# Optimization experiments

Hardware: AMD Instinct MI355X
Metric: run time of the kernel (lower is better)

## Reference

```python
import jax, jax.numpy as jnp
import numpy as np
from jax import lax

# --- geometry constants (match init_kwargs geo) ---
NVOX = (128, 128, 128)          # (nz, ny, nx) voxels
SVOX = (256.0, 256.0, 256.0)    # volume size in mm
NDET = (256, 256)               # (V, U) detector pixels
SDET = (512.0, 512.0)           # detector size in mm
DSO = 1000.0                    # source-to-isocenter distance
DSD = 1536.0                    # source-to-detector distance
N_ANGLES = 360


def setup_inputs() -> dict:
    key = jax.random.key(0)
    # projections: [B, 1, n_angles, nDetV, nDetU]
    x = jax.random.normal(key, (2, 1, N_ANGLES, NDET[0], NDET[1]), dtype=jnp.float32)
    return {"x": x}


def _backproject(proj):
    """Voxel-driven cone-beam back-projection (adjoint of cone-beam forward projector).

    proj: [B, A, V, U] projections over a circular source trajectory.
    returns volume [B, nz, ny, nx].
    """
    B, A, V, U = proj.shape
    nz, ny, nx = NVOX
    dz, dy, dx = SVOX[0] / nz, SVOX[1] / ny, SVOX[2] / nx
    dv, du = SDET[0] / V, SDET[1] / U

    # voxel center coordinates (isocenter at origin)
    zc = ((jnp.arange(nz, dtype=jnp.float32) - (nz - 1) / 2) * dz)[:, None, None]  # [nz,1,1]
    yc = ((jnp.arange(ny, dtype=jnp.float32) - (ny - 1) / 2) * dy)[None, :, None]  # [1,ny,1]
    xc = ((jnp.arange(nx, dtype=jnp.float32) - (nx - 1) / 2) * dx)[None, None, :]  # [1,1,nx]

    angles = jnp.linspace(0.0, 2.0 * np.pi, A, endpoint=False, dtype=jnp.float32)
    proj_a = jnp.moveaxis(proj, 1, 0)  # [A, B, V, U] for scan over angles

    def bilinear(p, iv, iu):
        # p: [B, V, U]; iv, iu: [nz, ny, nx] fractional detector coords
        valid = (iu >= 0) & (iu <= U - 1) & (iv >= 0) & (iv <= V - 1)
        iu = jnp.clip(iu, 0.0, U - 1.0)
        iv = jnp.clip(iv, 0.0, V - 1.0)
        u0 = jnp.floor(iu).astype(jnp.int32)
        v0 = jnp.floor(iv).astype(jnp.int32)
        u1 = jnp.minimum(u0 + 1, U - 1)
        v1 = jnp.minimum(v0 + 1, V - 1)
        fu = iu - u0
        fv = iv - v0
        s = (p[:, v0, u0] * ((1 - fv) * (1 - fu))
             + p[:, v0, u1] * ((1 - fv) * fu)
             + p[:, v1, u0] * (fv * (1 - fu))
             + p[:, v1, u1] * (fv * fu))            # [B,nz,ny,nx]
        return s * valid.astype(p.dtype)

    def body(vol, inp):
        theta, p = inp                                # scalar, [B,V,U]
        c, s = jnp.cos(theta), jnp.sin(theta)
        xr = xc * c + yc * s                          # rotated in-plane coords [1,ny,nx]
        yr = -xc * s + yc * c                         # [1,ny,nx]
        mag = DSD / (DSO - xr)                        # perspective magnification [1,ny,nx]
        iu = jnp.broadcast_to(yr * mag / du + (U - 1) / 2, (nz, ny, nx))
        iv = zc * mag / dv + (V - 1) / 2              # [nz,ny,nx]
        vol = vol + bilinear(p, iv, iu)
        return vol, None

    vol0 = jnp.zeros((B, nz, ny, nx), dtype=proj.dtype)
    vol, _ = lax.scan(body, vol0, (angles, proj_a))
    return vol


def reference(x):
    # x: [B, 1, A, V, U] -> volume [B, 1, nz, ny, nx]
    vol = _backproject(x[:, 0])
    return vol[:, None]
```

## Files before the change

### kernel.cpp

```cpp
#include <hip/hip_runtime.h>
#include <math.h>

#define NA    360
#define ZPT   8
#define CROWS 24
#define CPITCH 52
#define NCELLP 1280
#define VLO_MAX 231
#define ULO_MAX 204
#define BSTRIDE 94371840


typedef float v2f __attribute__((ext_vector_type(2)));
typedef __attribute__((address_space(1))) const void gas_t;
typedef __attribute__((address_space(3))) void las_t;

__device__ __forceinline__ int2 bbox_angle(float c, float s,
    float xclo, float xchi, float yclo, float ychi, float zvlo, float zvhi)
{
    const float a0 = xclo*c, a1 = xchi*c, b0 = yclo*s, b1 = ychi*s;
    const float xr0 = a0+b0, xr1 = a0+b1, xr2 = a1+b0, xr3 = a1+b1;
    const float xmn = fminf(fminf(xr0,xr1), fminf(xr2,xr3));
    const float xmx = fmaxf(fmaxf(xr0,xr1), fmaxf(xr2,xr3));
    const float c0 = yclo*c, c1 = ychi*c, d0 = xclo*s, d1 = xchi*s;
    const float yr0 = c0-d0, yr1 = c0-d1, yr2 = c1-d0, yr3 = c1-d1;
    const float ymn = fminf(fminf(yr0,yr1), fminf(yr2,yr3));
    const float ymx = fmaxf(fmaxf(yr0,yr1), fmaxf(yr2,yr3));
    const float mlo = 1536.f * __builtin_amdgcn_rcpf(1000.f - xmn);
    const float mhi = 1536.f * __builtin_amdgcn_rcpf(1000.f - xmx);
    const float umn = fminf(fminf(ymn*mlo, ymn*mhi), fminf(ymx*mlo, ymx*mhi));
    int u_lo = (int)floorf(fmaf(umn, 0.5f, 127.5f)) - 1;
    u_lo = u_lo < 0 ? 0 : (u_lo > ULO_MAX ? ULO_MAX : u_lo);
    const float vmn = fminf(fminf(zvlo*mlo, zvlo*mhi), fminf(zvhi*mlo, zvhi*mhi));
    int v_lo = (int)floorf(vmn + 127.5f) - 1;
    v_lo = v_lo < 0 ? 0 : (v_lo > VLO_MAX ? VLO_MAX : v_lo);
    return make_int2(u_lo, v_lo);
}

__device__ __forceinline__ void stage10(const char* gb, float* ldsw,
                                        const int goffB[10]) {
    #pragma unroll
    for (int i = 0; i < 10; ++i) {
        __builtin_amdgcn_global_load_lds(
            (gas_t*)(gb + goffB[i]),
            (las_t*)(ldsw + i * 64), 4, 0, 0);
    }
}

__device__ __forceinline__ void compute_angle(const v2f* __restrict__ smb,
    float c, float s, float xc, float yc, float zf0, int u_lo, int v_lo,
    v2f acc[ZPT])
{
    const float xr  = xc*c + yc*s;
    const float yr  = yc*c - xc*s;
    const float mag = 1536.f * __builtin_amdgcn_rcpf(1000.f - xr);
    const float iu  = fmaf(yr*mag, 0.5f, 127.5f);
    const bool uval = (iu >= 0.f) && (iu <= 255.f);
    const float iuc = fminf(fmaxf(iu, 0.f), 255.f);
    int u0 = (int)iuc; u0 = u0 > 254 ? 254 : u0;
    const float fu  = iuc - (float)u0;
    const float w   = uval ? 1.f : 0.f;
    const float wu1 = fu*w, wu0 = w - wu1;
    const v2f   w0v = {wu0, wu0};
    const v2f   w1v = {wu1, wu1};
    const int   ui  = u0 - u_lo;
    const float ivb = fmaf(zf0, mag, 127.5f) - (float)v_lo;
    #pragma unroll
    for (int k = 0; k < ZPT; ++k) {
        const float ivl = fmaf((float)k, mag, ivb);
        const int   v0  = (int)ivl;
        const float fv  = __builtin_amdgcn_fractf(ivl);
        const v2f* cell = smb + (v0 * CPITCH + ui);
        const v2f c00 = cell[0];
        const v2f c10 = cell[CPITCH];
        const v2f c01 = cell[1];
        const v2f c11 = cell[CPITCH+1];
        const v2f fvv = {fv, fv};
        const v2f q0 = __builtin_elementwise_fma(fvv, c10 - c00, c00);
        const v2f q1 = __builtin_elementwise_fma(fvv, c11 - c01, c01);
        acc[k] = __builtin_elementwise_fma(w0v, q0, acc[k]);
        acc[k] = __builtin_elementwise_fma(w1v, q1, acc[k]);
    }
}

__global__ __launch_bounds__(256, 4) void bp_kernel(const float* __restrict__ proj,
                                                    float* __restrict__ out) {
    __shared__ float2 cs_sh[NA];
    __shared__ int2   bb_sh[NA];
    __shared__ v2f    patch[2][NCELLP];

    const int tid = threadIdx.y * 16 + threadIdx.x;

    const int zg = blockIdx.x;
    const int t  = blockIdx.y;
    const int x0 = (t & 7) * 16;
    const int y0 = (t >> 3) * 16;
    const int zb = zg * ZPT;

    const float zf0  = (float)zb - 63.5f;
    const float xclo = ((float)x0 - 63.5f) * 2.f, xchi = xclo + 30.f;
    const float yclo = ((float)y0 - 63.5f) * 2.f, ychi = yclo + 30.f;

    for (int i = tid; i < NA; i += 256) {
        float th = (float)i * (float)(2.0 * M_PI / (double)NA);
        float sv, cv; sincosf(th, &sv, &cv);
        cs_sh[i] = make_float2(cv, sv);
        bb_sh[i] = bbox_angle(cv, sv, xclo, xchi, yclo, ychi, zf0, zf0 + 7.f);
    }
    __syncthreads();

    const int wv   = tid >> 6;
    const int lane = tid & 63;
    int goffB[10];
    #pragma unroll
    for (int i = 0; i < 10; ++i) {
        const int f    = wv * 640 + i * 64 + lane;
        const int bsel = f & 1;
        const int cidx = f >> 1;
        const int v    = cidx / 52;
        const int ucol = cidx - v * 52;
        goffB[i] = bsel * BSTRIDE + v * 1024 + ucol * 4;
    }

    const char* projB = (const char*)proj;
    const float xc = ((float)(x0 + threadIdx.x) - 63.5f) * 2.f;
    const float yc = ((float)(y0 + threadIdx.y) - 63.5f) * 2.f;

    float* l0 = (float*)&patch[0][0] + wv * 640;
    float* l1 = (float*)&patch[1][0] + wv * 640;

    v2f acc[ZPT];
    #pragma unroll
    for (int k = 0; k < ZPT; ++k) acc[k] = (v2f){0.f, 0.f};

    {
        const int2 lo = bb_sh[0];
        const uint32_t aoff = __builtin_amdgcn_readfirstlane(
            ((uint32_t)lo.y << 10) + ((uint32_t)lo.x << 2));
        stage10(projB + aoff, l0, goffB);
    }
    __syncthreads();

    for (int a = 0; a < NA; a += 2) {
        {
            const int2 lo = bb_sh[a + 1];
            const uint32_t aoff = __builtin_amdgcn_readfirstlane(
                (uint32_t)(a + 1) * 262144u +
                ((uint32_t)lo.y << 10) + ((uint32_t)lo.x << 2));
            stage10(projB + aoff, l1, goffB);
        }
        {
            const float2 cs = cs_sh[a];
            const int2   lo = bb_sh[a];
            compute_angle(patch[0], cs.x, cs.y, xc, yc, zf0, lo.x, lo.y, acc);
        }
        __syncthreads();
        if (a + 2 < NA) {
            const int2 lo = bb_sh[a + 2];
            const uint32_t aoff = __builtin_amdgcn_readfirstlane(
                (uint32_t)(a + 2) * 262144u +
                ((uint32_t)lo.y << 10) + ((uint32_t)lo.x << 2));
            stage10(projB + aoff, l0, goffB);
        }
        {
            const float2 cs = cs_sh[a + 1];
            const int2   lo = bb_sh[a + 1];
            compute_angle(patch[1], cs.x, cs.y, xc, yc, zf0, lo.x, lo.y, acc);
        }
        __syncthreads();
    }

    float* o0 = out + (((size_t)zb) * 128 + (y0 + threadIdx.y)) * 128
                    + (x0 + threadIdx.x);
    float* o1 = o0 + (size_t)128 * 128 * 128;
    #pragma unroll
    for (int k = 0; k < ZPT; ++k) {
        o0[(size_t)k * (128 * 128)] = acc[k].x;
        o1[(size_t)k * (128 * 128)] = acc[k].y;
    }
}

extern "C" void kernel_launch(void* const* d_in, const int* in_sizes, int n_in,
                              void* d_out, int out_size, void* d_ws, size_t ws_size,
                              hipStream_t stream) {
    const float* proj = (const float*)d_in[0];
    float* out = (float*)d_out;
    dim3 grid(128 / ZPT, 64, 1);
    dim3 block(16, 16, 1);
    hipLaunchKernelGGL(bp_kernel, grid, block, 0, stream, proj, out);
}
```

Baseline: 773.5 us.

## Deepen LDS prefetch pipeline to four buffers with one barrier per angle

```diff
diff --git a/kernel.cpp b/kernel.cpp
--- a/kernel.cpp
+++ b/kernel.cpp
@@ -83,11 +83,11 @@
     }
 }
 
-__global__ __launch_bounds__(256, 4) void bp_kernel(const float* __restrict__ proj,
+__global__ __launch_bounds__(256, 3) void bp_kernel(const float* __restrict__ proj,
                                                     float* __restrict__ out) {
     __shared__ float2 cs_sh[NA];
     __shared__ int2   bb_sh[NA];
-    __shared__ v2f    patch[2][NCELLP];
+    __shared__ v2f    patch[4][NCELLP];
 
     const int tid = threadIdx.y * 16 + threadIdx.x;
 
@@ -126,49 +126,39 @@
     const float xc = ((float)(x0 + threadIdx.x) - 63.5f) * 2.f;
     const float yc = ((float)(y0 + threadIdx.y) - 63.5f) * 2.f;
 
-    float* l0 = (float*)&patch[0][0] + wv * 640;
-    float* l1 = (float*)&patch[1][0] + wv * 640;
-
     v2f acc[ZPT];
     #pragma unroll
     for (int k = 0; k < ZPT; ++k) acc[k] = (v2f){0.f, 0.f};
 
-    {
-        const int2 lo = bb_sh[0];
+    #pragma unroll
+    for (int p = 0; p < 3; ++p) {
+        const int2 lo = bb_sh[p];
         const uint32_t aoff = __builtin_amdgcn_readfirstlane(
+            (uint32_t)p * 262144u +
             ((uint32_t)lo.y << 10) + ((uint32_t)lo.x << 2));
-        stage10(projB + aoff, l0, goffB);
+        stage10(projB + aoff, (float*)&patch[p][0] + wv * 640, goffB);
     }
-    __syncthreads();
 
-    for (int a = 0; a < NA; a += 2) {
+    for (int a = 0; a < NA; ++a) {
+        asm volatile("s_waitcnt vmcnt(20)" ::: "memory");
+        __builtin_amdgcn_s_barrier();
+
         {
-            const int2 lo = bb_sh[a + 1];
+            int an = a + 3; if (an >= NA) an -= NA;
+            const int2 lo = bb_sh[an];
             const uint32_t aoff = __builtin_amdgcn_readfirstlane(
-                (uint32_t)(a + 1) * 262144u +
+                (uint32_t)an * 262144u +
                 ((uint32_t)lo.y << 10) + ((uint32_t)lo.x << 2));
-            stage10(projB + aoff, l1, goffB);
+            stage10(projB + aoff, (float*)&patch[(a + 3) & 3][0] + wv * 640, goffB);
         }
         {
             const float2 cs = cs_sh[a];
             const int2   lo = bb_sh[a];
-            compute_angle(patch[0], cs.x, cs.y, xc, yc, zf0, lo.x, lo.y, acc);
+            compute_angle(patch[a & 3], cs.x, cs.y, xc, yc, zf0, lo.x, lo.y, acc);
         }
-        __syncthreads();
-        if (a + 2 < NA) {
-            const int2 lo = bb_sh[a + 2];
-            const uint32_t aoff = __builtin_amdgcn_readfirstlane(
-                (uint32_t)(a + 2) * 262144u +
-                ((uint32_t)lo.y << 10) + ((uint32_t)lo.x << 2));
-            stage10(projB + aoff, l0, goffB);
-        }
-        {
-            const float2 cs = cs_sh[a + 1];
-            const int2   lo = bb_sh[a + 1];
-            compute_angle(patch[1], cs.x, cs.y, xc, yc, zf0, lo.x, lo.y, acc);
-        }
-        __syncthreads();
     }
+
+    asm volatile("s_waitcnt vmcnt(0)" ::: "memory");
 
     float* o0 = out + (((size_t)zb) * 128 + (y0 + threadIdx.y)) * 128
                     + (x0 + threadIdx.x);
```

After: 1.004 ms. +29.8%, slower.
